# Kernel optimization log

Hardware: AMD Instinct MI355X
Metric: run time of the kernel (lower is better)

## Reference

```python
import jax, jax.numpy as jnp
import numpy as np
import math

D_MODEL = 2048
N_HEADS = 16
D_HEAD = D_MODEL // N_HEADS  # 128, also the RoPE dim
ROPE_BASE = 10000.0
B, T = 2, 2048


def _rope_cos_sin(seq_len, dim, dtype):
    inv_freq = 1.0 / (ROPE_BASE ** (jnp.arange(0, dim, 2, dtype=jnp.float32) / dim))
    t = jnp.arange(seq_len, dtype=jnp.float32)
    freqs = jnp.einsum('i,j->ij', t, inv_freq)          # [T, dim/2]
    emb = jnp.concatenate((freqs, freqs), axis=-1)       # [T, dim]  (half-concat layout, as in source)
    cos = jnp.cos(emb)[None, None, :, :].astype(dtype)   # [1,1,T,dim]
    sin = jnp.sin(emb)[None, None, :, :].astype(dtype)
    return cos, sin


def _apply_rot(x, cos, sin, dim):
    # interleaved pair rotation, faithful to the torch code
    x1 = x[..., 0:dim:2]
    x2 = x[..., 1:dim:2]
    x_rot = jnp.stack((-x2, x1), axis=-1).reshape(x.shape[:-1] + (dim,))
    return x[..., :dim] * cos + x_rot * sin


def setup_inputs() -> dict:
    key = jax.random.key(0)
    k1, k2, k3 = jax.random.split(key, 3)
    x = jax.random.normal(k1, (B, T, D_MODEL), dtype=jnp.float32)
    # causal additive mask, broadcastable to [B,H,T,T]
    neg = jnp.finfo(jnp.float32).min / 2
    causal = jnp.triu(jnp.full((T, T), neg, dtype=jnp.float32), k=1)
    mask = causal[None, None, :, :]
    Wqkv = jax.random.normal(k2, (D_MODEL, 3 * D_MODEL), dtype=jnp.float32) * (1.0 / math.sqrt(D_MODEL))
    bqkv = jnp.zeros((3 * D_MODEL,), dtype=jnp.float32)
    Wo = jax.random.normal(k3, (D_MODEL, D_MODEL), dtype=jnp.float32) * (1.0 / math.sqrt(D_MODEL))
    bo = jnp.zeros((D_MODEL,), dtype=jnp.float32)
    return {"x": x, "mask": mask, "Wqkv": Wqkv, "bqkv": bqkv, "Wo": Wo, "bo": bo}


def reference(x, mask, Wqkv, bqkv, Wo, bo):
    Bx, Tx, C = x.shape
    qkv = x @ Wqkv + bqkv                                     # [B,T,3C]
    qkv = qkv.reshape(Bx, Tx, 3, N_HEADS, D_HEAD)
    qkv = jnp.transpose(qkv, (2, 0, 3, 1, 4))                 # [3,B,H,T,dh]
    q, k, v = qkv[0], qkv[1], qkv[2]
    cos, sin = _rope_cos_sin(Tx, D_HEAD, x.dtype)
    q = _apply_rot(q, cos, sin, D_HEAD)
    k = _apply_rot(k, cos, sin, D_HEAD)
    att = jnp.einsum('bhqd,bhkd->bhqk', q, k) / math.sqrt(D_HEAD)
    att = att + mask
    att = jax.nn.softmax(att, axis=-1)
    y = jnp.einsum('bhqk,bhkd->bhqd', att, v)                 # [B,H,T,dh]
    y = jnp.transpose(y, (0, 2, 1, 3)).reshape(Bx, Tx, C)
    return y @ Wo + bo
```

## Files before the change

### kernel.cpp

```cpp
#include <hip/hip_runtime.h>
#include <stdint.h>

#define TDIM 2048
#define DMODEL 2048
#define NHEADS 16
#define DHEAD 128
#define NBATCH 2
#define NTOK (NBATCH * TDIM)
#define NQKV (3 * DMODEL)
#define BHTOT (NBATCH * NHEADS)

typedef unsigned short u16;
typedef __attribute__((ext_vector_type(8))) short bf16x8;
typedef __attribute__((ext_vector_type(4))) float f32x4;
typedef __attribute__((ext_vector_type(4))) int i32x4;

__device__ __forceinline__ u16 f2bf(float f) {
  union { float f; uint32_t u; } v; v.f = f;
  uint32_t u = v.u + 0x7fffu + ((v.u >> 16) & 1u);
  return (u16)(u >> 16);
}
__device__ __forceinline__ float bf2f(u16 h) {
  union { uint32_t u; float f; } v; v.u = ((uint32_t)h) << 16;
  return v.f;
}

#define GLOAD16(g, l)                                                        \
  __builtin_amdgcn_global_load_lds(                                          \
      (const __attribute__((address_space(1))) void*)(g),                    \
      (__attribute__((address_space(3))) void*)(l), 16, 0, 0)

__global__ void rope_table_kernel(float* __restrict__ ct, float* __restrict__ st) {
  int idx = blockIdx.x * 256 + threadIdx.x;
  int t = idx >> 6, m = idx & 63;
  float inv = expf(-(float)m * (9.210340371976184f / 64.0f));
  float ang = (float)t * inv;
  ct[idx] = cosf(ang);
  st[idx] = sinf(ang);
}

__global__ void convert_kernel(const float* __restrict__ in, u16* __restrict__ out) {
  int i = blockIdx.x * 256 + threadIdx.x;
  float4 v = ((const float4*)in)[i];
  ushort4 o;
  o.x = f2bf(v.x); o.y = f2bf(v.y); o.z = f2bf(v.z); o.w = f2bf(v.w);
  ((ushort4*)out)[i] = o;
}

__global__ __launch_bounds__(256) void transpose_convert_kernel(
    const float* __restrict__ in, u16* __restrict__ out, int K, int N) {
  __shared__ u16 tile[32][33];
  int n0 = blockIdx.x * 32, k0 = blockIdx.y * 32;
  int tx = threadIdx.x, ty = threadIdx.y;
  #pragma unroll
  for (int q = 0; q < 4; q++) {
    int k = ty + q * 8;
    tile[k][tx] = f2bf(in[(size_t)(k0 + k) * N + n0 + tx]);
  }
  __syncthreads();
  #pragma unroll
  for (int q = 0; q < 4; q++) {
    int n = ty + q * 8;
    out[(size_t)(n0 + n) * K + k0 + tx] = tile[tx][n];
  }
}

__global__ __launch_bounds__(256) void vtrans_kernel(
    const u16* __restrict__ Vtmp, u16* __restrict__ Vt) {
  __shared__ u16 tile[32][33];
  int bh = blockIdx.z;
  int t0 = blockIdx.x * 32, d0 = blockIdx.y * 32;
  int tx = threadIdx.x, ty = threadIdx.y;
  const u16* src = Vtmp + (size_t)bh * TDIM * DHEAD;
  u16* dst = Vt + (size_t)bh * DHEAD * TDIM;
  #pragma unroll
  for (int q = 0; q < 4; q++) {
    int t = ty + q * 8;
    tile[t][tx] = src[(size_t)(t0 + t) * DHEAD + d0 + tx];
  }
  __syncthreads();
  #pragma unroll
  for (int q = 0; q < 4; q++) {
    int d = ty + q * 8;
    dst[(size_t)(d0 + d) * TDIM + t0 + tx] = tile[tx][d];
  }
}

template <int MODE>
__global__ __launch_bounds__(512, 2) void gemm_bt_kernel(
    const u16* __restrict__ A, const u16* __restrict__ Bt,
    const float* __restrict__ bias,
    u16* __restrict__ q_out, u16* __restrict__ k_out, u16* __restrict__ v_out,
    float* __restrict__ f_out,
    const float* __restrict__ ct, const float* __restrict__ st, int K) {
  __shared__ __attribute__((aligned(128))) char lds[2][49152];
  const int tid = threadIdx.x;
  const int lane = tid & 63, w = tid >> 6;
  const int wr = w >> 2, wc = w & 3;
  const int g = lane >> 4, c = lane & 15;

  const int gx = gridDim.x;
  const int nwg = gx * gridDim.y;
  const int lin = (int)blockIdx.x + (int)blockIdx.y * gx;
  const int swz = (lin & 7) * (nwg >> 3) + (lin >> 3);
  const int m0 = (swz % gx) * 128, n0 = (swz / gx) * 256;

  const size_t rowb = (size_t)K * 2;
  const int NKT = K >> 6;

  const char* aSrc[2]; int aDst[2];
  const char* bSrc[4]; int bDst[4];
  #pragma unroll
  for (int p = 0; p < 2; p++) {
    int o = p * 8192 + tid * 16;
    int row = o >> 7, j = (o >> 4) & 7;
    aSrc[p] = (const char*)A + (size_t)(m0 + row) * rowb + ((j ^ (row & 7)) << 4);
    aDst[p] = o;
  }
  #pragma unroll
  for (int p = 0; p < 4; p++) {
    int o = p * 8192 + tid * 16;
    int row = o >> 7, j = (o >> 4) & 7;
    bSrc[p] = (const char*)Bt + (size_t)(n0 + row) * rowb + ((j ^ (row & 7)) << 4);
    bDst[p] = 16384 + o;
  }

#define STAGE(bufp, kt)                                                      \
  {                                                                          \
    const size_t kb_ = (size_t)(kt) * 128;                                   \
    _Pragma("unroll") for (int p_ = 0; p_ < 2; p_++)                         \
        GLOAD16(aSrc[p_] + kb_, (bufp) + aDst[p_]);                          \
    _Pragma("unroll") for (int p_ = 0; p_ < 4; p_++)                         \
        GLOAD16(bSrc[p_] + kb_, (bufp) + bDst[p_]);                          \
  }

  int aRd[4][2], bRd[4][2];
  #pragma unroll
  for (int m = 0; m < 4; m++) {
    #pragma unroll
    for (int ks = 0; ks < 2; ks++) {
      int arow = wr * 64 + m * 16 + c;
      aRd[m][ks] = arow * 128 + (((ks * 4 + g) ^ (c & 7)) << 4);
      int brow = wc * 64 + m * 16 + c;
      bRd[m][ks] = 16384 + brow * 128 + (((ks * 4 + g) ^ (c & 7)) << 4);
    }
  }

  const f32x4 zero = {0.f, 0.f, 0.f, 0.f};
  f32x4 acc[4][4];
  #pragma unroll
  for (int m = 0; m < 4; m++)
    #pragma unroll
    for (int n = 0; n < 4; n++) acc[m][n] = zero;

  STAGE(lds[0], 0);
  STAGE(lds[1], 1);
  asm volatile("s_waitcnt vmcnt(6)" ::: "memory");
  __builtin_amdgcn_s_barrier();
  __builtin_amdgcn_sched_barrier(0);

  for (int kt = 0; kt < NKT; kt++) {
    char* bp = lds[kt & 1];
    bf16x8 bfr[4][2], afr[2][2], af2[2][2];
    #pragma unroll
    for (int n = 0; n < 4; n++)
      #pragma unroll
      for (int ks = 0; ks < 2; ks++)
        bfr[n][ks] = *(const bf16x8*)(bp + bRd[n][ks]);
    #pragma unroll
    for (int m = 0; m < 2; m++)
      #pragma unroll
      for (int ks = 0; ks < 2; ks++)
        afr[m][ks] = *(const bf16x8*)(bp + aRd[m][ks]);
    __builtin_amdgcn_s_setprio(1);
    #pragma unroll
    for (int ks = 0; ks < 2; ks++)
      #pragma unroll
      for (int m = 0; m < 2; m++)
        #pragma unroll
        for (int n = 0; n < 4; n++)
          acc[m][n] = __builtin_amdgcn_mfma_f32_16x16x32_bf16(
              afr[m][ks], bfr[n][ks], acc[m][n], 0, 0, 0);
    __builtin_amdgcn_s_setprio(0);

    #pragma unroll
    for (int m = 0; m < 2; m++)
      #pragma unroll
      for (int ks = 0; ks < 2; ks++)
        af2[m][ks] = *(const bf16x8*)(bp + aRd[m + 2][ks]);
    asm volatile("s_waitcnt lgkmcnt(0)" ::: "memory");
    __builtin_amdgcn_s_barrier();
    __builtin_amdgcn_sched_barrier(0);
    if (kt + 2 < NKT) STAGE(bp, kt + 2);
    __builtin_amdgcn_s_setprio(1);
    #pragma unroll
    for (int ks = 0; ks < 2; ks++)
      #pragma unroll
      for (int m = 0; m < 2; m++)
        #pragma unroll
        for (int n = 0; n < 4; n++)
          acc[m + 2][n] = __builtin_amdgcn_mfma_f32_16x16x32_bf16(
              af2[m][ks], bfr[n][ks], acc[m + 2][n], 0, 0, 0);
    __builtin_amdgcn_s_setprio(0);

    if (kt < NKT - 1) {
      if (kt + 2 < NKT) {
        asm volatile("s_waitcnt vmcnt(6)" ::: "memory");
      } else {
        asm volatile("s_waitcnt vmcnt(0)" ::: "memory");
      }
      __builtin_amdgcn_s_barrier();
      __builtin_amdgcn_sched_barrier(0);
    }
  }
#undef STAGE

  #pragma unroll
  for (int m = 0; m < 4; m++) {
    #pragma unroll
    for (int n = 0; n < 4; n++) {
      int gcol = n0 + wc * 64 + n * 16 + c;
      float bv = bias[gcol];
      float val[4];
      #pragma unroll
      for (int r = 0; r < 4; r++) val[r] = acc[m][n][r] + bv;
      if (MODE == 0) {
        int s = n0 >> 11;
        int rem = gcol & 2047;
        int h = rem >> 7, d = rem & 127;
        int b0 = (m0 + wr * 64 + m * 16) >> 11;
        size_t hb = (((size_t)(b0 * NHEADS + h)) * TDIM) * DHEAD + d;
        if (s == 2) {
          #pragma unroll
          for (int r = 0; r < 4; r++) {
            int t = (m0 + wr * 64 + m * 16 + g * 4 + r) & (TDIM - 1);
            v_out[hb + (size_t)t * DHEAD] = f2bf(val[r]);
          }
        } else {
          int mf = gcol & 63;
          float sgn = (c & 1) ? 1.0f : -1.0f;
          u16* dst = (s == 0) ? q_out : k_out;
          float qs = (s == 0) ? 0.08838834764831845f : 1.0f;
          #pragma unroll
          for (int r = 0; r < 4; r++) {
            float part = __shfl_xor(val[r], 1, 64);
            int t = (m0 + wr * 64 + m * 16 + g * 4 + r) & (TDIM - 1);
            float cs = ct[t * 64 + mf], sn = st[t * 64 + mf];
            float rot = (val[r] * cs + sgn * part * sn) * qs;
            dst[hb + (size_t)t * DHEAD] = f2bf(rot);
          }
        }
      } else {
        #pragma unroll
        for (int r = 0; r < 4; r++) {
          int grow = m0 + wr * 64 + m * 16 + g * 4 + r;
          f_out[(size_t)grow * DMODEL + gcol] = val[r];
        }
      }
    }
  }
}

__global__ __launch_bounds__(256) void attn_kernel(
    const u16* __restrict__ Q, const u16* __restrict__ K,
    const u16* __restrict__ Vt, u16* __restrict__ Yattn) {
  __shared__ u16 Ks[2][64 * 128];
  __shared__ u16 Vs[2][128 * 64];
  __shared__ u16 Ps[4][16 * 64];
  const int tid = threadIdx.x, lane = tid & 63, w = tid >> 6;
  const int g = lane >> 4, c = lane & 15;
  const int bh = blockIdx.y, b = bh >> 4, h = bh & 15;
  const u16* Qp = Q + (size_t)bh * TDIM * DHEAD;
  const u16* Kp = K + (size_t)bh * TDIM * DHEAD;
  const u16* Vp = Vt + (size_t)bh * DHEAD * TDIM;
  const f32x4 zero = {0.f, 0.f, 0.f, 0.f};

  for (int half = 0; half < 2; half++) {
    const int qt = half ? (31 - (int)blockIdx.x) : (int)blockIdx.x;
    const int qb = qt * 64 + w * 16;

    bf16x8 qf[4];
    #pragma unroll
    for (int kc = 0; kc < 4; kc++)
      qf[kc] = *(const bf16x8*)(Qp + (size_t)(qb + c) * DHEAD + kc * 32 + g * 8);

    f32x4 po[8];
    #pragma unroll
    for (int df = 0; df < 8; df++) po[df] = zero;
    float mrun[4], lrun[4];
    #pragma unroll
    for (int r = 0; r < 4; r++) { mrun[r] = -1e30f; lrun[r] = 0.f; }

    const int nt = qt + 1;

    {
      #pragma unroll
      for (int p = 0; p < 4; p++) {
        int off = p * 4096 + tid * 16;
        int kr = off >> 8, kc4 = (off & 255) >> 4;
        GLOAD16((const char*)Kp + (size_t)kr * 256 + ((kc4 ^ (kr & 7)) << 4),
                (char*)Ks[0] + off);
        int vr = off >> 7, vc4 = (off & 127) >> 4;
        GLOAD16((const char*)Vp + (size_t)vr * (TDIM * 2) + ((vc4 ^ (vr & 7)) << 4),
                (char*)Vs[0] + off);
      }
    }
    __syncthreads();

    int cur = 0;
    for (int t = 0; t < nt; t++) {
      if (t + 1 < nt) {
        int kv0n = (t + 1) * 64;
        char* KsN = (char*)Ks[cur ^ 1];
        char* VsN = (char*)Vs[cur ^ 1];
        #pragma unroll
        for (int p = 0; p < 4; p++) {
          int off = p * 4096 + tid * 16;
          int kr = off >> 8, kc4 = (off & 255) >> 4;
          GLOAD16((const char*)Kp + (size_t)(kv0n + kr) * 256 +
                      ((kc4 ^ (kr & 7)) << 4),
                  KsN + off);
          int vr = off >> 7, vc4 = (off & 127) >> 4;
          GLOAD16((const char*)Vp + (size_t)vr * (TDIM * 2) + (size_t)kv0n * 2 +
                      ((vc4 ^ (vr & 7)) << 4),
                  VsN + off);
        }
      }

      const u16* KsC = Ks[cur];
      const u16* VsC = Vs[cur];
      const int kv0 = t * 64;

      f32x4 sa[4];
      #pragma unroll
      for (int n = 0; n < 4; n++) sa[n] = zero;
      __builtin_amdgcn_s_setprio(1);
      #pragma unroll
      for (int n = 0; n < 4; n++) {
        int krow = n * 16 + c;
        #pragma unroll
        for (int kc = 0; kc < 4; kc++) {
          int kb = (kc * 32 + g * 8) * 2;
          bf16x8 kf = *(const bf16x8*)((const char*)KsC + krow * 256 +
                                       (kb ^ ((krow & 7) << 4)));
          sa[n] = __builtin_amdgcn_mfma_f32_16x16x32_bf16(qf[kc], kf, sa[n], 0, 0, 0);
        }
      }
      __builtin_amdgcn_s_setprio(0);

      if (kv0 + 63 > qb) {
        #pragma unroll
        for (int n = 0; n < 4; n++) {
          int col = kv0 + n * 16 + c;
          #pragma unroll
          for (int r = 0; r < 4; r++) {
            int qrow = qb + g * 4 + r;
            if (col > qrow) sa[n][r] = -1e30f;
          }
        }
      }

      float pvals[4][4];
      #pragma unroll
      for (int r = 0; r < 4; r++) {
        float vmax = fmaxf(fmaxf(sa[0][r], sa[1][r]), fmaxf(sa[2][r], sa[3][r]));
        #pragma unroll
        for (int d = 1; d < 16; d <<= 1) vmax = fmaxf(vmax, __shfl_xor(vmax, d, 64));
        float mnew = fmaxf(mrun[r], vmax);
        float scale = __expf(mrun[r] - mnew);
        float rs = 0.f;
        #pragma unroll
        for (int n = 0; n < 4; n++) {
          float p = __expf(sa[n][r] - mnew);
          pvals[r][n] = p;
          rs += p;
        }
        #pragma unroll
        for (int d = 1; d < 16; d <<= 1) rs += __shfl_xor(rs, d, 64);
        lrun[r] = lrun[r] * scale + rs;
        mrun[r] = mnew;
        #pragma unroll
        for (int df = 0; df < 8; df++) po[df][r] *= scale;
      }

      char* Pw = (char*)&Ps[w][0];
      #pragma unroll
      for (int r = 0; r < 4; r++) {
        int ri = g * 4 + r;
        #pragma unroll
        for (int n = 0; n < 4; n++) {
          int colb = (n * 16 + c) * 2;
          *(u16*)(Pw + ri * 128 + (colb ^ ((ri & 7) << 4))) = f2bf(pvals[r][n]);
        }
      }
      bf16x8 pa[2];
      #pragma unroll
      for (int kc2 = 0; kc2 < 2; kc2++) {
        int pb = (kc2 * 32 + g * 8) * 2;
        pa[kc2] = *(const bf16x8*)(Pw + c * 128 + (pb ^ ((c & 7) << 4)));
      }
      __builtin_amdgcn_s_setprio(1);
      #pragma unroll
      for (int df = 0; df < 8; df++) {
        #pragma unroll
        for (int kc2 = 0; kc2 < 2; kc2++) {
          int vrow = df * 16 + c;
          int vb = (kc2 * 32 + g * 8) * 2;
          bf16x8 vf = *(const bf16x8*)((const char*)VsC + vrow * 128 +
                                       (vb ^ ((vrow & 7) << 4)));
          po[df] = __builtin_amdgcn_mfma_f32_16x16x32_bf16(pa[kc2], vf, po[df], 0, 0, 0);
        }
      }
      __builtin_amdgcn_s_setprio(0);

      __syncthreads();
      cur ^= 1;
    }

    float inv[4];
    #pragma unroll
    for (int r = 0; r < 4; r++) inv[r] = 1.0f / lrun[r];
    #pragma unroll
    for (int df = 0; df < 8; df++) {
      #pragma unroll
      for (int r = 0; r < 4; r++) {
        int trow = qb + g * 4 + r;
        int col = h * DHEAD + df * 16 + c;
        Yattn[((size_t)b * TDIM + trow) * DMODEL + col] = f2bf(po[df][r] * inv[r]);
      }
    }
  }
}

extern "C" void kernel_launch(void* const* d_in, const int* in_sizes, int n_in,
                              void* d_out, int out_size, void* d_ws, size_t ws_size,
                              hipStream_t stream) {
  const float* x    = (const float*)d_in[0];
  const float* Wqkv = (const float*)d_in[2];
  const float* bqkv = (const float*)d_in[3];
  const float* Wo   = (const float*)d_in[4];
  const float* bo   = (const float*)d_in[5];
  float* out = (float*)d_out;

  char* ws = (char*)d_ws;
  size_t o = 0;
  u16* xb    = (u16*)(ws + o); o += (size_t)NTOK * DMODEL * 2;
  u16* Wqkvt = (u16*)(ws + o); o += (size_t)NQKV * DMODEL * 2;
  u16* Wot   = (u16*)(ws + o); o += (size_t)DMODEL * DMODEL * 2;
  u16* Qb    = (u16*)(ws + o); o += (size_t)BHTOT * TDIM * DHEAD * 2;
  u16* Kb    = (u16*)(ws + o); o += (size_t)BHTOT * TDIM * DHEAD * 2;
  u16* Vtmp  = (u16*)(ws + o); o += (size_t)BHTOT * TDIM * DHEAD * 2;
  float* ct  = (float*)(ws + o); o += (size_t)TDIM * 64 * 4;
  float* st  = (float*)(ws + o); o += (size_t)TDIM * 64 * 4;
  u16* Vt    = xb;
  u16* Yattn = Vtmp;

  dim3 tb32x8(32, 8);

  rope_table_kernel<<<(TDIM * 64) / 256, 256, 0, stream>>>(ct, st);
  convert_kernel<<<(NTOK * DMODEL / 4) / 256, 256, 0, stream>>>(x, xb);
  transpose_convert_kernel<<<dim3(NQKV / 32, DMODEL / 32), tb32x8, 0, stream>>>(
      Wqkv, Wqkvt, DMODEL, NQKV);
  transpose_convert_kernel<<<dim3(DMODEL / 32, DMODEL / 32), tb32x8, 0, stream>>>(
      Wo, Wot, DMODEL, DMODEL);

  gemm_bt_kernel<0><<<dim3(NTOK / 128, NQKV / 256), 512, 0, stream>>>(
      xb, Wqkvt, bqkv, Qb, Kb, Vtmp, nullptr, ct, st, DMODEL);

  vtrans_kernel<<<dim3(TDIM / 32, DHEAD / 32, BHTOT), tb32x8, 0, stream>>>(Vtmp, Vt);

  attn_kernel<<<dim3(16, BHTOT), 256, 0, stream>>>(Qb, Kb, Vt, Yattn);

  gemm_bt_kernel<1><<<dim3(NTOK / 128, DMODEL / 256), 512, 0, stream>>>(
      Yattn, Wot, bo, nullptr, nullptr, nullptr, out, nullptr, nullptr, DMODEL);
}
```

Baseline: 298.1 us.

## Single-buffer attention K/V LDS with split staged loads; drop GEMM tile swizzle

The attention kernel goes from double-buffered K and V shared-memory tiles to single buffers. The next K tile is loaded during softmax and the next V tile after the PV MFMAs, with explicit vmcnt waits and barriers. This halves K/V LDS usage, likely to raise occupancy, but exposes the V load latency at each iteration end and adds barriers. Separately, the GEMM drops its workgroup index swizzle for plain blockIdx tiling, which may hurt L2 locality.

```diff
diff --git a/kernel.cpp b/kernel.cpp
--- a/kernel.cpp
+++ b/kernel.cpp
@@ -98,13 +98,7 @@
   const int lane = tid & 63, w = tid >> 6;
   const int wr = w >> 2, wc = w & 3;
   const int g = lane >> 4, c = lane & 15;
-
-  const int gx = gridDim.x;
-  const int nwg = gx * gridDim.y;
-  const int lin = (int)blockIdx.x + (int)blockIdx.y * gx;
-  const int swz = (lin & 7) * (nwg >> 3) + (lin >> 3);
-  const int m0 = (swz % gx) * 128, n0 = (swz / gx) * 256;
-
+  const int m0 = blockIdx.x * 128, n0 = blockIdx.y * 256;
   const size_t rowb = (size_t)K * 2;
   const int NKT = K >> 6;
 
@@ -264,8 +258,8 @@
 __global__ __launch_bounds__(256) void attn_kernel(
     const u16* __restrict__ Q, const u16* __restrict__ K,
     const u16* __restrict__ Vt, u16* __restrict__ Yattn) {
-  __shared__ u16 Ks[2][64 * 128];
-  __shared__ u16 Vs[2][128 * 64];
+  __shared__ u16 Ks[64 * 128];
+  __shared__ u16 Vs[128 * 64];
   __shared__ u16 Ps[4][16 * 64];
   const int tid = threadIdx.x, lane = tid & 63, w = tid >> 6;
   const int g = lane >> 4, c = lane & 15;
@@ -275,6 +269,28 @@
   const u16* Vp = Vt + (size_t)bh * DHEAD * TDIM;
   const f32x4 zero = {0.f, 0.f, 0.f, 0.f};
 
+
+#define STAGE_K(kv0)                                                         \
+  {                                                                          \
+    _Pragma("unroll") for (int p_ = 0; p_ < 4; p_++) {                       \
+      int off = p_ * 4096 + tid * 16;                                        \
+      int kr = off >> 8, kc4 = (off & 255) >> 4;                             \
+      GLOAD16((const char*)Kp + (size_t)((kv0) + kr) * 256 +                 \
+                  ((kc4 ^ (kr & 7)) << 4),                                   \
+              (char*)Ks + off);                                              \
+    }                                                                        \
+  }
+#define STAGE_V(kv0)                                                         \
+  {                                                                          \
+    _Pragma("unroll") for (int p_ = 0; p_ < 4; p_++) {                       \
+      int off = p_ * 4096 + tid * 16;                                        \
+      int vr = off >> 7, vc4 = (off & 127) >> 4;                             \
+      GLOAD16((const char*)Vp + (size_t)vr * (TDIM * 2) + (size_t)(kv0) * 2 +\
+                  ((vc4 ^ (vr & 7)) << 4),                                   \
+              (char*)Vs + off);                                              \
+    }                                                                        \
+  }
+
   for (int half = 0; half < 2; half++) {
     const int qt = half ? (31 - (int)blockIdx.x) : (int)blockIdx.x;
     const int qb = qt * 64 + w * 16;
@@ -293,43 +309,15 @@
 
     const int nt = qt + 1;
 
-    {
-      #pragma unroll
-      for (int p = 0; p < 4; p++) {
-        int off = p * 4096 + tid * 16;
-        int kr = off >> 8, kc4 = (off & 255) >> 4;
-        GLOAD16((const char*)Kp + (size_t)kr * 256 + ((kc4 ^ (kr & 7)) << 4),
-                (char*)Ks[0] + off);
-        int vr = off >> 7, vc4 = (off & 127) >> 4;
-        GLOAD16((const char*)Vp + (size_t)vr * (TDIM * 2) + ((vc4 ^ (vr & 7)) << 4),
-                (char*)Vs[0] + off);
-      }
-    }
-    __syncthreads();
-
-    int cur = 0;
+    STAGE_K(0);
+    STAGE_V(0);
+    asm volatile("s_waitcnt vmcnt(4)" ::: "memory");
+    __builtin_amdgcn_s_barrier();
+    __builtin_amdgcn_sched_barrier(0);
+
     for (int t = 0; t < nt; t++) {
-      if (t + 1 < nt) {
-        int kv0n = (t + 1) * 64;
-        char* KsN = (char*)Ks[cur ^ 1];
-        char* VsN = (char*)Vs[cur ^ 1];
-        #pragma unroll
-        for (int p = 0; p < 4; p++) {
-          int off = p * 4096 + tid * 16;
-          int kr = off >> 8, kc4 = (off & 255) >> 4;
-          GLOAD16((const char*)Kp + (size_t)(kv0n + kr) * 256 +
-                      ((kc4 ^ (kr & 7)) << 4),
-                  KsN + off);
-          int vr = off >> 7, vc4 = (off & 127) >> 4;
-          GLOAD16((const char*)Vp + (size_t)vr * (TDIM * 2) + (size_t)kv0n * 2 +
-                      ((vc4 ^ (vr & 7)) << 4),
-                  VsN + off);
-        }
-      }
-
-      const u16* KsC = Ks[cur];
-      const u16* VsC = Vs[cur];
       const int kv0 = t * 64;
+      const bool more = (t + 1 < nt);
 
       f32x4 sa[4];
       #pragma unroll
@@ -341,7 +329,7 @@
         #pragma unroll
         for (int kc = 0; kc < 4; kc++) {
           int kb = (kc * 32 + g * 8) * 2;
-          bf16x8 kf = *(const bf16x8*)((const char*)KsC + krow * 256 +
+          bf16x8 kf = *(const bf16x8*)((const char*)Ks + krow * 256 +
                                        (kb ^ ((krow & 7) << 4)));
           sa[n] = __builtin_amdgcn_mfma_f32_16x16x32_bf16(qf[kc], kf, sa[n], 0, 0, 0);
         }
@@ -360,6 +348,10 @@
         }
       }
 
+      asm volatile("s_waitcnt lgkmcnt(0)" ::: "memory");
+      __builtin_amdgcn_s_barrier();
+      if (more) STAGE_K(kv0 + 64);
+
       float pvals[4][4];
       #pragma unroll
       for (int r = 0; r < 4; r++) {
@@ -383,6 +375,14 @@
         for (int df = 0; df < 8; df++) po[df][r] *= scale;
       }
 
+      if (more) {
+        asm volatile("s_waitcnt vmcnt(4)" ::: "memory");
+      } else {
+        asm volatile("s_waitcnt vmcnt(0)" ::: "memory");
+      }
+      __builtin_amdgcn_s_barrier();
+      __builtin_amdgcn_sched_barrier(0);
+
       char* Pw = (char*)&Ps[w][0];
       #pragma unroll
       for (int r = 0; r < 4; r++) {
@@ -406,15 +406,21 @@
         for (int kc2 = 0; kc2 < 2; kc2++) {
           int vrow = df * 16 + c;
           int vb = (kc2 * 32 + g * 8) * 2;
-          bf16x8 vf = *(const bf16x8*)((const char*)VsC + vrow * 128 +
+          bf16x8 vf = *(const bf16x8*)((const char*)Vs + vrow * 128 +
                                        (vb ^ ((vrow & 7) << 4)));
           po[df] = __builtin_amdgcn_mfma_f32_16x16x32_bf16(pa[kc2], vf, po[df], 0, 0, 0);
         }
       }
       __builtin_amdgcn_s_setprio(0);
 
-      __syncthreads();
-      cur ^= 1;
+      asm volatile("s_waitcnt lgkmcnt(0)" ::: "memory");
+      __builtin_amdgcn_s_barrier();
+      if (more) {
+        STAGE_V(kv0 + 64);
+        asm volatile("s_waitcnt vmcnt(4)" ::: "memory");
+      }
+      __builtin_amdgcn_s_barrier();
+      __builtin_amdgcn_sched_barrier(0);
     }
 
     float inv[4];
@@ -430,6 +436,8 @@
       }
     }
   }
+#undef STAGE_K
+#undef STAGE_V
 }
 
 extern "C" void kernel_launch(void* const* d_in, const int* in_sizes, int n_in,
```

Result: no change. 296.9 us (-0.4%).
